# Kernel optimization log

Measured on AMD Instinct MI355X. Metric: run time of the kernel, lower is better.

## Reference

```python
import jax, jax.numpy as jnp
import numpy as np


def setup_inputs() -> dict:
    key = jax.random.key(0)
    k1, k2, k3 = jax.random.split(key, 3)
    N, E, D = 10000, 160000, 512
    x = jax.random.normal(k1, (N, D), dtype=jnp.float32)
    edge_index = jax.random.randint(k2, (2, E), 0, N, dtype=jnp.int64)
    W = jax.random.normal(k3, (D, D), dtype=jnp.float32) * (1.0 / np.sqrt(D))
    b = jnp.zeros((D,), dtype=jnp.float32)
    return {"x": x, "edge_index": edge_index, "W": W, "b": b}


def reference(x, edge_index, W, b):
    # PyG GCNConv: add self-loops, symmetric deg^-1/2 normalization,
    # linear transform (no bias in lin), scatter-add aggregate, then + bias.
    N = x.shape[0]
    loop = jnp.arange(N, dtype=edge_index.dtype)
    src = jnp.concatenate([edge_index[0], loop])  # message sources (j)
    dst = jnp.concatenate([edge_index[1], loop])  # message targets (i)
    deg = jax.ops.segment_sum(jnp.ones(src.shape, dtype=x.dtype), dst, num_segments=N)
    deg_inv_sqrt = jnp.where(deg > 0, jax.lax.rsqrt(deg), 0.0)
    norm = deg_inv_sqrt[src] * deg_inv_sqrt[dst]  # [E+N]
    h = x @ W  # [N, D] linear transform
    msg = h[src] * norm[:, None]  # gather + scale, [E+N, D]
    out = jax.ops.segment_sum(msg, dst, num_segments=N) + b
    return out
```

## Files before the change

kernel.cpp:

```cpp
#include <hip/hip_runtime.h>
#include <stdint.h>


#define D_DIM 512
#define SLOTS 64

typedef _Float16 half8 __attribute__((ext_vector_type(8)));
typedef float floatx4 __attribute__((ext_vector_type(4)));

__global__ __launch_bounds__(256) void fused_pre_kernel(const float* __restrict__ W,
                                                        const int* __restrict__ src,
                                                        const int* __restrict__ dst,
                                                        _Float16* __restrict__ Bt,
                                                        int* __restrict__ cursor,
                                                        int* __restrict__ csr,
                                                        int E) {
    __shared__ float tile[32][33];
    int bid = blockIdx.x;
    if (bid < 256) {
        int k0 = (bid & 15) * 32, n0 = (bid >> 4) * 32;
        int tx = threadIdx.x & 31, ty = threadIdx.x >> 5;
        #pragma unroll
        for (int r = ty; r < 32; r += 8)
            tile[r][tx] = W[(size_t)(k0 + r) * D_DIM + n0 + tx];
        __syncthreads();
        #pragma unroll
        for (int r = ty; r < 32; r += 8)
            Bt[(size_t)(n0 + r) * D_DIM + k0 + tx] = (_Float16)tile[tx][r];
        return;
    }
    int e = (bid - 256) * 256 + threadIdx.x;
    if (e < E) {
        int d = dst[e];
        int pos = atomicAdd(&cursor[d], 1);
        if (pos < SLOTS) csr[(d << 6) + pos] = src[e];
    }
}

#define GBM 64
#define GBN 128
#define GBK 32
#define LDK 40

__global__ __launch_bounds__(256) void gemm_kernel(const float* __restrict__ X,
                                                   const _Float16* __restrict__ Bt,
                                                   const int* __restrict__ cursor,
                                                   _Float16* __restrict__ pre,
                                                   int M, int ngb) {
    __shared__ _Float16 Asl[2][GBM * LDK];
    __shared__ _Float16 Bsl[2][GBN * LDK];

    int tid  = threadIdx.x;
    int lane = tid & 63;
    int wave = tid >> 6;
    int wr = wave >> 1, wc = wave & 1;

    int rowbase = (blockIdx.x % ngb) * GBM;
    int colbase = (blockIdx.x / ngb) * GBN;

    int s_r = tid >> 2;
    int s_k = (tid & 3) << 3;

    int fm = lane & 15;
    int fk = (lane >> 4) << 3;

    int ar0 = rowbase + s_r; if (ar0 >= M) ar0 = M - 1;
    const float* px0 = X + (size_t)ar0 * D_DIM + s_k;
    const _Float16* pb0 = Bt + (size_t)(colbase + s_r) * D_DIM + s_k;
    const _Float16* pb1 = Bt + (size_t)(colbase + s_r + 64) * D_DIM + s_k;

    floatx4 acc[2][4];
    #pragma unroll
    for (int i = 0; i < 2; ++i)
        #pragma unroll
        for (int j = 0; j < 4; ++j)
            #pragma unroll
            for (int e = 0; e < 4; ++e)
                acc[i][j][e] = 0.f;

    float4 xa0 = *(const float4*)px0, xb0 = *(const float4*)(px0 + 4);
    half8 bv0 = *(const half8*)pb0;
    half8 bv1 = *(const half8*)pb1;
    half8 av0;
    av0[0] = (_Float16)xa0.x; av0[1] = (_Float16)xa0.y; av0[2] = (_Float16)xa0.z; av0[3] = (_Float16)xa0.w;
    av0[4] = (_Float16)xb0.x; av0[5] = (_Float16)xb0.y; av0[6] = (_Float16)xb0.z; av0[7] = (_Float16)xb0.w;
    *(half8*)(&Asl[0][s_r * LDK + s_k])        = av0;
    *(half8*)(&Bsl[0][s_r * LDK + s_k])        = bv0;
    *(half8*)(&Bsl[0][(s_r + 64) * LDK + s_k]) = bv1;

    const int KT = D_DIM / GBK;
    for (int kt = 0; kt < KT; ++kt) {
        int buf = kt & 1;
        __syncthreads();

        if (kt + 1 < KT) {
            int ko = (kt + 1) * GBK;
            xa0 = *(const float4*)(px0 + ko); xb0 = *(const float4*)(px0 + ko + 4);
            bv0 = *(const half8*)(pb0 + ko);
            bv1 = *(const half8*)(pb1 + ko);
        }

        half8 afrag[2], bfrag[4];
        #pragma unroll
        for (int t = 0; t < 2; ++t)
            afrag[t] = *(const half8*)(&Asl[buf][(wr * 32 + t * 16 + fm) * LDK + fk]);
        #pragma unroll
        for (int t = 0; t < 4; ++t)
            bfrag[t] = *(const half8*)(&Bsl[buf][(wc * 64 + t * 16 + fm) * LDK + fk]);
        #pragma unroll
        for (int i = 0; i < 2; ++i)
            #pragma unroll
            for (int j = 0; j < 4; ++j)
                acc[i][j] = __builtin_amdgcn_mfma_f32_16x16x32_f16(afrag[i], bfrag[j], acc[i][j], 0, 0, 0);

        if (kt + 1 < KT) {
            int nb = buf ^ 1;
            av0[0] = (_Float16)xa0.x; av0[1] = (_Float16)xa0.y; av0[2] = (_Float16)xa0.z; av0[3] = (_Float16)xa0.w;
            av0[4] = (_Float16)xb0.x; av0[5] = (_Float16)xb0.y; av0[6] = (_Float16)xb0.z; av0[7] = (_Float16)xb0.w;
            *(half8*)(&Asl[nb][s_r * LDK + s_k])        = av0;
            *(half8*)(&Bsl[nb][s_r * LDK + s_k])        = bv0;
            *(half8*)(&Bsl[nb][(s_r + 64) * LDK + s_k]) = bv1;
        }
    }

    int mrow0 = (lane >> 4) << 2;
    #pragma unroll
    for (int i = 0; i < 2; ++i) {
        #pragma unroll
        for (int r = 0; r < 4; ++r) {
            int row = rowbase + wr * 32 + i * 16 + mrow0 + r;
            if (row < M) {
                float sc = rsqrtf((float)cursor[row] + 1.0f);
                #pragma unroll
                for (int j = 0; j < 4; ++j) {
                    int col = colbase + wc * 64 + j * 16 + fm;
                    pre[(size_t)row * D_DIM + col] = (_Float16)(acc[i][j][r] * sc);
                }
            }
        }
    }
}

__global__ __launch_bounds__(256) void gather_kernel(const _Float16* __restrict__ pre,
                                                     const int* __restrict__ csr,
                                                     const int* __restrict__ cursor,
                                                     const float* __restrict__ b,
                                                     float* __restrict__ out, int N) {
    int wave = threadIdx.x >> 6;
    int lane = threadIdx.x & 63;
    int node = blockIdx.x * 4 + wave;
    if (node >= N) return;
    int c8 = lane << 3;

    int cnt = cursor[node];
    int end = cnt < SLOTS ? cnt : SLOTS;
    float di = rsqrtf((float)cnt + 1.0f);
    const int* lst = csr + (node << 6);

    float acc[8];
    {
        half8 self = *(const half8*)(pre + (size_t)node * D_DIM + c8);
        #pragma unroll
        for (int e = 0; e < 8; ++e) acc[e] = (float)self[e];
    }

    int j = 0;
    for (; j + 7 < end; j += 8) {
        half8 v[8];
        #pragma unroll
        for (int u = 0; u < 8; ++u) {
            int s = lst[j + u];
            v[u] = *(const half8*)(pre + (size_t)s * D_DIM + c8);
        }
        #pragma unroll
        for (int e = 0; e < 8; ++e) {
            float t = 0.f;
            #pragma unroll
            for (int u = 0; u < 8; ++u) t += (float)v[u][e];
            acc[e] += t;
        }
    }
    for (; j + 3 < end; j += 4) {
        half8 v[4];
        #pragma unroll
        for (int u = 0; u < 4; ++u) {
            int s = lst[j + u];
            v[u] = *(const half8*)(pre + (size_t)s * D_DIM + c8);
        }
        #pragma unroll
        for (int e = 0; e < 8; ++e)
            acc[e] += (float)v[0][e] + (float)v[1][e] + (float)v[2][e] + (float)v[3][e];
    }
    for (; j < end; ++j) {
        int s = lst[j];
        half8 v0 = *(const half8*)(pre + (size_t)s * D_DIM + c8);
        #pragma unroll
        for (int e = 0; e < 8; ++e) acc[e] += (float)v0[e];
    }

    float4 b0 = *(const float4*)(b + c8);
    float4 b1 = *(const float4*)(b + c8 + 4);
    floatx4 o0, o1;
    o0[0] = b0.x + di * acc[0];
    o0[1] = b0.y + di * acc[1];
    o0[2] = b0.z + di * acc[2];
    o0[3] = b0.w + di * acc[3];
    o1[0] = b1.x + di * acc[4];
    o1[1] = b1.y + di * acc[5];
    o1[2] = b1.z + di * acc[6];
    o1[3] = b1.w + di * acc[7];
    __builtin_nontemporal_store(o0, (floatx4*)(out + (size_t)node * D_DIM + c8));
    __builtin_nontemporal_store(o1, (floatx4*)(out + (size_t)node * D_DIM + c8 + 4));
}

extern "C" void kernel_launch(void* const* d_in, const int* in_sizes, int n_in,
                              void* d_out, int out_size, void* d_ws, size_t ws_size,
                              hipStream_t stream) {
    const float* x  = (const float*)d_in[0];
    const int*   ei = (const int*)d_in[1];
    const float* W  = (const float*)d_in[2];
    const float* b  = (const float*)d_in[3];
    float* out = (float*)d_out;

    int N = in_sizes[0] / D_DIM;
    int E = in_sizes[1] / 2;
    const int* src = ei;
    const int* dst = ei + E;

    char* ws = (char*)d_ws;
    size_t prebytes = (size_t)N * D_DIM * sizeof(_Float16);
    size_t btbytes  = (size_t)D_DIM * D_DIM * sizeof(_Float16);
    int Npad = (N + 256) & ~255;
    _Float16* pre  = (_Float16*)ws;
    _Float16* Bt   = (_Float16*)(ws + prebytes);
    int*      cursor = (int*)(ws + prebytes + btbytes);
    int*      csr    = cursor + Npad;

    (void)hipMemsetAsync(cursor, 0, (size_t)N * sizeof(int), stream);

    int degb = (E + 255) / 256;
    fused_pre_kernel<<<256 + degb, 256, 0, stream>>>(W, src, dst, Bt, cursor, csr, E);

    int ngb = (N + GBM - 1) / GBM;
    gemm_kernel<<<ngb * (D_DIM / GBN), 256, 0, stream>>>(x, Bt, cursor, pre, N, ngb);

    gather_kernel<<<(N + 3) / 4, 256, 0, stream>>>(pre, csr, cursor, b, out, N);
}
```

Measured before the change: 127.8 us.

## Fuse CSR build into GEMM launch and move source normalization into gather

Drops the memset by zeroing the degree counters inside the weight-transpose prep kernel. Moves the edge-bucketing atomics into extra blocks of the GEMM launch, so graph construction runs alongside the matmul. This is possible because the GEMM no longer scales rows by the source degree. That scaling now happens in the gather, which reads the cursor value for each neighbour and applies its rsqrt, adding a small extra load and multiply per edge. The goal is to remove a launch and overlap the atomic scatter with compute.

Measured after the change: 125.2 us. 2.0% less time.

```diff
diff --git a/kernel.cpp b/kernel.cpp
--- a/kernel.cpp
+++ b/kernel.cpp
@@ -8,33 +8,24 @@
 typedef _Float16 half8 __attribute__((ext_vector_type(8)));
 typedef float floatx4 __attribute__((ext_vector_type(4)));
 
-__global__ __launch_bounds__(256) void fused_pre_kernel(const float* __restrict__ W,
-                                                        const int* __restrict__ src,
-                                                        const int* __restrict__ dst,
-                                                        _Float16* __restrict__ Bt,
-                                                        int* __restrict__ cursor,
-                                                        int* __restrict__ csr,
-                                                        int E) {
+__global__ __launch_bounds__(256) void prep_kernel(const float* __restrict__ W,
+                                                   _Float16* __restrict__ Bt,
+                                                   int* __restrict__ cursor,
+                                                   int N) {
     __shared__ float tile[32][33];
     int bid = blockIdx.x;
-    if (bid < 256) {
-        int k0 = (bid & 15) * 32, n0 = (bid >> 4) * 32;
-        int tx = threadIdx.x & 31, ty = threadIdx.x >> 5;
-        #pragma unroll
-        for (int r = ty; r < 32; r += 8)
-            tile[r][tx] = W[(size_t)(k0 + r) * D_DIM + n0 + tx];
-        __syncthreads();
-        #pragma unroll
-        for (int r = ty; r < 32; r += 8)
-            Bt[(size_t)(n0 + r) * D_DIM + k0 + tx] = (_Float16)tile[tx][r];
-        return;
-    }
-    int e = (bid - 256) * 256 + threadIdx.x;
-    if (e < E) {
-        int d = dst[e];
-        int pos = atomicAdd(&cursor[d], 1);
-        if (pos < SLOTS) csr[(d << 6) + pos] = src[e];
-    }
+    int gtid = bid * 256 + threadIdx.x;
+    if (gtid < N) cursor[gtid] = 0;
+
+    int k0 = (bid & 15) * 32, n0 = (bid >> 4) * 32;
+    int tx = threadIdx.x & 31, ty = threadIdx.x >> 5;
+    #pragma unroll
+    for (int r = ty; r < 32; r += 8)
+        tile[r][tx] = W[(size_t)(k0 + r) * D_DIM + n0 + tx];
+    __syncthreads();
+    #pragma unroll
+    for (int r = ty; r < 32; r += 8)
+        Bt[(size_t)(n0 + r) * D_DIM + k0 + tx] = (_Float16)tile[tx][r];
 }
 
 #define GBM 64
@@ -44,11 +35,24 @@
 
 __global__ __launch_bounds__(256) void gemm_kernel(const float* __restrict__ X,
                                                    const _Float16* __restrict__ Bt,
-                                                   const int* __restrict__ cursor,
                                                    _Float16* __restrict__ pre,
-                                                   int M, int ngb) {
+                                                   const int* __restrict__ src,
+                                                   const int* __restrict__ dst,
+                                                   int* __restrict__ cursor,
+                                                   int* __restrict__ csr,
+                                                   int M, int E, int ngb, int gemm_blocks) {
     __shared__ _Float16 Asl[2][GBM * LDK];
     __shared__ _Float16 Bsl[2][GBN * LDK];
+
+    if (blockIdx.x >= (unsigned)gemm_blocks) {
+        int e = (blockIdx.x - gemm_blocks) * 256 + threadIdx.x;
+        if (e < E) {
+            int d = dst[e];
+            int pos = atomicAdd(&cursor[d], 1);
+            if (pos < SLOTS) csr[(d << 6) + pos] = src[e];
+        }
+        return;
+    }
 
     int tid  = threadIdx.x;
     int lane = tid & 63;
@@ -130,11 +134,10 @@
         for (int r = 0; r < 4; ++r) {
             int row = rowbase + wr * 32 + i * 16 + mrow0 + r;
             if (row < M) {
-                float sc = rsqrtf((float)cursor[row] + 1.0f);
                 #pragma unroll
                 for (int j = 0; j < 4; ++j) {
                     int col = colbase + wc * 64 + j * 16 + fm;
-                    pre[(size_t)row * D_DIM + col] = (_Float16)(acc[i][j][r] * sc);
+                    pre[(size_t)row * D_DIM + col] = (_Float16)acc[i][j][r];
                 }
             }
         }
@@ -161,41 +164,47 @@
     {
         half8 self = *(const half8*)(pre + (size_t)node * D_DIM + c8);
         #pragma unroll
-        for (int e = 0; e < 8; ++e) acc[e] = (float)self[e];
+        for (int e = 0; e < 8; ++e) acc[e] = di * (float)self[e];
     }
 
     int j = 0;
     for (; j + 7 < end; j += 8) {
         half8 v[8];
+        float dv[8];
         #pragma unroll
         for (int u = 0; u < 8; ++u) {
             int s = lst[j + u];
             v[u] = *(const half8*)(pre + (size_t)s * D_DIM + c8);
+            dv[u] = rsqrtf((float)cursor[s] + 1.0f);
         }
         #pragma unroll
         for (int e = 0; e < 8; ++e) {
             float t = 0.f;
             #pragma unroll
-            for (int u = 0; u < 8; ++u) t += (float)v[u][e];
+            for (int u = 0; u < 8; ++u) t += dv[u] * (float)v[u][e];
             acc[e] += t;
         }
     }
     for (; j + 3 < end; j += 4) {
         half8 v[4];
+        float dv[4];
         #pragma unroll
         for (int u = 0; u < 4; ++u) {
             int s = lst[j + u];
             v[u] = *(const half8*)(pre + (size_t)s * D_DIM + c8);
+            dv[u] = rsqrtf((float)cursor[s] + 1.0f);
         }
         #pragma unroll
         for (int e = 0; e < 8; ++e)
-            acc[e] += (float)v[0][e] + (float)v[1][e] + (float)v[2][e] + (float)v[3][e];
+            acc[e] += dv[0] * (float)v[0][e] + dv[1] * (float)v[1][e]
+                    + dv[2] * (float)v[2][e] + dv[3] * (float)v[3][e];
     }
     for (; j < end; ++j) {
         int s = lst[j];
         half8 v0 = *(const half8*)(pre + (size_t)s * D_DIM + c8);
-        #pragma unroll
-        for (int e = 0; e < 8; ++e) acc[e] += (float)v0[e];
+        float dv = rsqrtf((float)cursor[s] + 1.0f);
+        #pragma unroll
+        for (int e = 0; e < 8; ++e) acc[e] += dv * (float)v0[e];
     }
 
     float4 b0 = *(const float4*)(b + c8);
@@ -236,13 +245,13 @@
     int*      cursor = (int*)(ws + prebytes + btbytes);
     int*      csr    = cursor + Npad;
 
-    (void)hipMemsetAsync(cursor, 0, (size_t)N * sizeof(int), stream);
-
+    prep_kernel<<<256, 256, 0, stream>>>(W, Bt, cursor, N);
+
+    int ngb = (N + GBM - 1) / GBM;
+    int gemm_blocks = ngb * (D_DIM / GBN);
     int degb = (E + 255) / 256;
-    fused_pre_kernel<<<256 + degb, 256, 0, stream>>>(W, src, dst, Bt, cursor, csr, E);
-
-    int ngb = (N + GBM - 1) / GBM;
-    gemm_kernel<<<ngb * (D_DIM / GBN), 256, 0, stream>>>(x, Bt, cursor, pre, N, ngb);
+    gemm_kernel<<<gemm_blocks + degb, 256, 0, stream>>>(x, Bt, pre, src, dst,
+                                                        cursor, csr, N, E, ngb, gemm_blocks);
 
     gather_kernel<<<(N + 3) / 4, 256, 0, stream>>>(pre, csr, cursor, b, out, N);
 }
```
